# Optimization experiments

Hardware: AMD Instinct MI355X
Metric: run time of the kernel (lower is better)

Reference implementation:

```python
import jax, jax.numpy as jnp
import numpy as np

B = 64
C = 384
HEADS = 6
HD = 64
MLP = 1536
LAYERS = 12
PATCH = 16
IMG = 224
GRID = IMG // PATCH  # 14
NPATCH = GRID * GRID  # 196
NCLS = 100
EPS = 1e-6
PRUNE = {2: 0.1, 4: 0.15, 6: 0.2}
SCALE = HD ** -0.5


def layer_norm(x, g, b):
    m = jnp.mean(x, axis=-1, keepdims=True)
    v = jnp.var(x, axis=-1, keepdims=True)
    return (x - m) * jax.lax.rsqrt(v + EPS) * g + b


def attention(x, qkv_w, qkv_b, proj_w, proj_b):
    # x: [B, N, C]; weights stored as [in, out]
    Bn, N, _ = x.shape
    qkv = x @ qkv_w + qkv_b                      # [B, N, 3C]
    qkv = qkv.reshape(Bn, N, 3, HEADS, HD).transpose(2, 0, 3, 1, 4)
    q, k, v = qkv[0], qkv[1], qkv[2]             # [B, H, N, HD]
    attn = jax.nn.softmax(jnp.einsum('bhnd,bhmd->bhnm', q, k) * SCALE, axis=-1)
    out = jnp.einsum('bhnm,bhmd->bhnd', attn, v)
    out = out.transpose(0, 2, 1, 3).reshape(Bn, N, C)
    return out @ proj_w + proj_b, attn


def mlp(x, fc1_w, fc1_b, fc2_w, fc2_b):
    h = jax.nn.gelu(x @ fc1_w + fc1_b, approximate=False)
    return h @ fc2_w + fc2_b


def prune(x, attn, ratio):
    # x: [B, N, C]; attn: [B, H, N, N]
    scores = attn[:, :, 0, 1:].mean(axis=1)      # CLS attention to tokens, head-avg [B, N-1]
    keep = int(scores.shape[1] * (1 - ratio))
    _, idx = jax.lax.top_k(scores, keep)         # [B, keep], descending score order (matches torch.topk)
    tokens = jnp.take_along_axis(x[:, 1:, :], idx[:, :, None], axis=1)
    return jnp.concatenate([x[:, :1, :], tokens], axis=1)


def patch_embed(x, patch_w, patch_b):
    # 16x16 stride-16 conv == patchify + matmul. x: [B, 3, 224, 224]
    Bn = x.shape[0]
    p = x.reshape(Bn, 3, GRID, PATCH, GRID, PATCH).transpose(0, 2, 4, 1, 3, 5)
    p = p.reshape(Bn, NPATCH, 3 * PATCH * PATCH)
    return p @ patch_w + patch_b


def setup_inputs() -> dict:
    key = jax.random.key(0)
    ks = jax.random.split(key, 10)
    s = 0.02
    d = {}
    d['x'] = jax.random.normal(ks[0], (B, 3, IMG, IMG), jnp.float32)
    d['patch_w'] = jax.random.normal(ks[1], (3 * PATCH * PATCH, C), jnp.float32) * s
    d['patch_b'] = jnp.zeros((C,), jnp.float32)
    d['cls_token'] = jax.random.normal(ks[2], (1, 1, C), jnp.float32) * s
    d['pos_embed'] = jax.random.normal(ks[3], (1, NPATCH + 1, C), jnp.float32) * s
    d['ln1_g'] = jnp.ones((LAYERS, C), jnp.float32)
    d['ln1_b'] = jnp.zeros((LAYERS, C), jnp.float32)
    d['qkv_w'] = jax.random.normal(ks[4], (LAYERS, C, 3 * C), jnp.float32) * s
    d['qkv_b'] = jnp.zeros((LAYERS, 3 * C), jnp.float32)
    d['proj_w'] = jax.random.normal(ks[5], (LAYERS, C, C), jnp.float32) * s
    d['proj_b'] = jnp.zeros((LAYERS, C), jnp.float32)
    d['ln2_g'] = jnp.ones((LAYERS, C), jnp.float32)
    d['ln2_b'] = jnp.zeros((LAYERS, C), jnp.float32)
    d['fc1_w'] = jax.random.normal(ks[6], (LAYERS, C, MLP), jnp.float32) * s
    d['fc1_b'] = jnp.zeros((LAYERS, MLP), jnp.float32)
    d['fc2_w'] = jax.random.normal(ks[7], (LAYERS, MLP, C), jnp.float32) * s
    d['fc2_b'] = jnp.zeros((LAYERS, C), jnp.float32)
    d['norm_g'] = jnp.ones((C,), jnp.float32)
    d['norm_b'] = jnp.zeros((C,), jnp.float32)
    d['head_w'] = jax.random.normal(ks[8], (C, NCLS), jnp.float32) * s
    d['head_b'] = jnp.zeros((NCLS,), jnp.float32)
    return d


def reference(x, patch_w, patch_b, cls_token, pos_embed, ln1_g, ln1_b, qkv_w, qkv_b,
              proj_w, proj_b, ln2_g, ln2_b, fc1_w, fc1_b, fc2_w, fc2_b,
              norm_g, norm_b, head_w, head_b):
    Bn = x.shape[0]
    h = patch_embed(x, patch_w, patch_b)                          # [B, 196, C]
    cls = jnp.broadcast_to(cls_token, (Bn, 1, C))
    h = jnp.concatenate([cls, h], axis=1) + pos_embed             # [B, 197, C]
    for i in range(LAYERS):
        y, attn = attention(layer_norm(h, ln1_g[i], ln1_b[i]),
                            qkv_w[i], qkv_b[i], proj_w[i], proj_b[i])
        h = h + y
        if i in PRUNE:
            h = prune(h, attn, PRUNE[i])
        h = h + mlp(layer_norm(h, ln2_g[i], ln2_b[i]),
                    fc1_w[i], fc1_b[i], fc2_w[i], fc2_b[i])
    h = layer_norm(h, norm_g, norm_b)
    return h[:, 0] @ head_w + head_b                              # [B, NCLS]
```

## Files before the change

### kernel.cpp

```cpp
#include <hip/hip_runtime.h>
#include <hip/hip_bf16.h>
#include <math.h>

#define BATCH 64
#define CDIM 384
#define NHEADS 6
#define HD 64
#define MLPD 1536
#define NLAYERS 12
#define NPATCH 196
#define NTOK0 197
#define NCLS 100

typedef unsigned short ushortT;
typedef __attribute__((ext_vector_type(8))) short short8v;
typedef __attribute__((ext_vector_type(4))) float float4v;

__device__ inline ushortT f2b(float f) {
  union { float f; unsigned u; } x; x.f = f;
  unsigned r = x.u + 0x7fffu + ((x.u >> 16) & 1u);
  return (ushortT)(r >> 16);
}
__device__ inline float b2f(ushortT u) {
  union { unsigned u; float f; } x; x.u = ((unsigned)u) << 16;
  return x.f;
}

__device__ inline void gload_lds16(const ushortT* g, ushortT* l) {
  __builtin_amdgcn_global_load_lds((const __attribute__((address_space(1))) void*)g,
                                   (__attribute__((address_space(3))) void*)l, 16, 0, 0);
}

__device__ inline float wave_sum(float v) {
  #pragma unroll
  for (int o = 32; o > 0; o >>= 1) v += __shfl_xor(v, o);
  return v;
}

__global__ __launch_bounds__(256) void im2col_bf16(const float* __restrict__ x, ushortT* __restrict__ P) {
  int i = blockIdx.x * 256 + threadIdx.x;
  const int total = BATCH * NPATCH * 768;
  if (i >= total) return;
  int k = i % 768;
  int row = i / 768;
  int c = k >> 8;
  int r = k & 255;
  int py = r >> 4, px = r & 15;
  int b = row / NPATCH;
  int p = row % NPATCH;
  int gy = p / 14, gx = p % 14;
  P[i] = f2b(x[(((size_t)b * 3 + c) * 224 + gy * 16 + py) * 224 + gx * 16 + px]);
}

__global__ __launch_bounds__(256) void assemble_kernel(const float* __restrict__ patchout,
                                                       const float* __restrict__ cls_tok,
                                                       const float* __restrict__ pos,
                                                       float* __restrict__ h) {
  int i = blockIdx.x * 256 + threadIdx.x;
  const int total = BATCH * NTOK0 * CDIM;
  if (i >= total) return;
  int c = i % CDIM;
  int n = (i / CDIM) % NTOK0;
  int b = i / (CDIM * NTOK0);
  float v = (n == 0) ? cls_tok[c] : patchout[((size_t)b * NPATCH + (n - 1)) * CDIM + c];
  h[i] = v + pos[n * CDIM + c];
}

__global__ __launch_bounds__(256) void wtrans_layer(const float* __restrict__ qkv_w, const float* __restrict__ proj_w,
                                                    const float* __restrict__ fc1_w, const float* __restrict__ fc2_w,
                                                    ushortT* __restrict__ wq, ushortT* __restrict__ wp,
                                                    ushortT* __restrict__ w1, ushortT* __restrict__ w2) {
  int id = blockIdx.x;
  const float* W; ushortT* O; int K, N, t;
  if (id < 432)       { W = qkv_w; O = wq; K = 384;  N = 1152; t = id; }
  else if (id < 576)  { W = proj_w; O = wp; K = 384; N = 384;  t = id - 432; }
  else if (id < 1152) { W = fc1_w; O = w1; K = 384;  N = 1536; t = id - 576; }
  else                { W = fc2_w; O = w2; K = 1536; N = 384;  t = id - 1152; }
  int tilesK = K >> 5;
  int k0 = (t % tilesK) << 5, n0 = (t / tilesK) << 5;
  __shared__ float tile[32][33];
  int tx = threadIdx.x & 31, ty = threadIdx.x >> 5;
  #pragma unroll
  for (int i = 0; i < 4; ++i)
    tile[ty + 8 * i][tx] = W[(size_t)(k0 + ty + 8 * i) * N + n0 + tx];
  __syncthreads();
  #pragma unroll
  for (int i = 0; i < 4; ++i)
    O[(size_t)(n0 + ty + 8 * i) * K + k0 + tx] = f2b(tile[tx][ty + 8 * i]);
}

__global__ __launch_bounds__(256) void wtrans_one(const float* __restrict__ W, ushortT* __restrict__ O, int K, int N) {
  int t = blockIdx.x;
  int tilesK = K >> 5;
  int k0 = (t % tilesK) << 5, n0 = (t / tilesK) << 5;
  __shared__ float tile[32][33];
  int tx = threadIdx.x & 31, ty = threadIdx.x >> 5;
  #pragma unroll
  for (int i = 0; i < 4; ++i)
    tile[ty + 8 * i][tx] = W[(size_t)(k0 + ty + 8 * i) * N + n0 + tx];
  __syncthreads();
  #pragma unroll
  for (int i = 0; i < 4; ++i)
    O[(size_t)(n0 + ty + 8 * i) * K + k0 + tx] = f2b(tile[tx][ty + 8 * i]);
}

template<int ACT, int RES, int OBF>
__global__ __launch_bounds__(256) void gemm_mfma(const ushortT* __restrict__ A, const ushortT* __restrict__ Wt,
                                                 const float* __restrict__ bias, const float* __restrict__ res,
                                                 void* __restrict__ outp, int M, int N, int K) {
  __shared__ __align__(16) ushortT Asl[128 * 32];
  __shared__ __align__(16) ushortT Bsl[128 * 32];
  const int tid = threadIdx.x;
  const int lane = tid & 63, wave = tid >> 6;
  const int wr = wave >> 1, wc = wave & 1;
  const int bm = blockIdx.y * 128, bn = blockIdx.x * 128;
  float4v acc[4][4] = {};

  const int srow = wave * 16 + (lane >> 2);
  const int scol = (lane & 3) * 8;
  const ushortT* ag0 = A + (size_t)(bm + srow) * K + scol;
  const ushortT* ag1 = A + (size_t)(bm + 64 + srow) * K + scol;
  const ushortT* bg0 = Wt + (size_t)(bn + srow) * K + scol;
  const ushortT* bg1 = Wt + (size_t)(bn + 64 + srow) * K + scol;
  ushortT* ldsA0 = &Asl[wave * 512];
  ushortT* ldsA1 = &Asl[2048 + wave * 512];
  ushortT* ldsB0 = &Bsl[wave * 512];
  ushortT* ldsB1 = &Bsl[2048 + wave * 512];

  const int fr = lane & 15, g8 = (lane >> 4) * 8;

  for (int k0 = 0; k0 < K; k0 += 32) {
    gload_lds16(ag0 + k0, ldsA0);
    gload_lds16(ag1 + k0, ldsA1);
    gload_lds16(bg0 + k0, ldsB0);
    gload_lds16(bg1 + k0, ldsB1);
    __syncthreads();
    short8v af[4], bf[4];
    #pragma unroll
    for (int i = 0; i < 4; ++i) {
      af[i] = *(const short8v*)&Asl[(wr * 64 + i * 16 + fr) * 32 + g8];
      bf[i] = *(const short8v*)&Bsl[(wc * 64 + i * 16 + fr) * 32 + g8];
    }
    #pragma unroll
    for (int i = 0; i < 4; ++i)
      #pragma unroll
      for (int j = 0; j < 4; ++j)
        acc[i][j] = __builtin_amdgcn_mfma_f32_16x16x32_bf16(af[i], bf[j], acc[i][j], 0, 0, 0);
    __syncthreads();
  }

  const int c0 = lane & 15;
  const int r4 = (lane >> 4) * 4;
  #pragma unroll
  for (int i = 0; i < 4; ++i) {
    #pragma unroll
    for (int j = 0; j < 4; ++j) {
      const int col = bn + wc * 64 + j * 16 + c0;
      #pragma unroll
      for (int q = 0; q < 4; ++q) {
        const int row = bm + wr * 64 + i * 16 + r4 + q;
        if (row < M) {
          float v = acc[i][j][q] + bias[col];
          if (ACT == 1) v = 0.5f * v * (1.0f + erff(v * 0.70710678118654752f));
          if (RES) v += res[(size_t)row * N + col];
          if (OBF) ((ushortT*)outp)[(size_t)row * N + col] = f2b(v);
          else     ((float*)outp)[(size_t)row * N + col] = v;
        }
      }
    }
  }
}

__global__ __launch_bounds__(256) void ln_bf16(const float* __restrict__ in, ushortT* __restrict__ out,
                                               const float* __restrict__ g, const float* __restrict__ bb,
                                               int rows) {
  const int r = blockIdx.x * 4 + (threadIdx.x >> 6);
  if (r >= rows) return;
  const int t = threadIdx.x & 63;
  const float* xr = in + (size_t)r * CDIM;
  ushortT* orow = out + (size_t)r * CDIM;
  float v[6];
  float s = 0.f;
  #pragma unroll
  for (int i = 0; i < 6; ++i) { v[i] = xr[i * 64 + t]; s += v[i]; }
  s = wave_sum(s);
  float mean = s * (1.0f / CDIM);
  float q = 0.f;
  #pragma unroll
  for (int i = 0; i < 6; ++i) { float d = v[i] - mean; q += d * d; }
  q = wave_sum(q);
  float rstd = rsqrtf(q * (1.0f / CDIM) + 1e-6f);
  #pragma unroll
  for (int i = 0; i < 6; ++i) {
    int c = i * 64 + t;
    orow[c] = f2b((v[i] - mean) * rstd * g[c] + bb[c]);
  }
}

__global__ __launch_bounds__(64) void ln_kernel(const float* __restrict__ in, float* __restrict__ out,
                                                const float* __restrict__ g, const float* __restrict__ bb,
                                                int rows, size_t in_stride, size_t out_stride) {
  int r = blockIdx.x;
  if (r >= rows) return;
  const float* xr = in + (size_t)r * in_stride;
  float* orow = out + (size_t)r * out_stride;
  int t = threadIdx.x;
  float v[6];
  float s = 0.f;
  #pragma unroll
  for (int i = 0; i < 6; ++i) { v[i] = xr[i * 64 + t]; s += v[i]; }
  s = wave_sum(s);
  float mean = s * (1.0f / CDIM);
  float q = 0.f;
  #pragma unroll
  for (int i = 0; i < 6; ++i) { float d = v[i] - mean; q += d * d; }
  q = wave_sum(q);
  float rstd = rsqrtf(q * (1.0f / CDIM) + 1e-6f);
  #pragma unroll
  for (int i = 0; i < 6; ++i) {
    int c = i * 64 + t;
    orow[c] = (v[i] - mean) * rstd * g[c] + bb[c];
  }
}

template<int KS>
__global__ __launch_bounds__(256) void attn3(const ushortT* __restrict__ qkv, ushortT* __restrict__ attnout,
                                             float* __restrict__ cls_attn, int N) {
  constexpr int NT = 2 * KS;
  constexpr int KT = 32 * KS;
  const int h = blockIdx.y, b = blockIdx.z;
  const int rb = blockIdx.x * 64;
  const int tid = threadIdx.x;
  const int w = tid >> 6, l = tid & 63;
  const int c = l & 15, g = l >> 4;

  __shared__ __align__(16) ushortT Vt[64][232];
  __shared__ __align__(16) ushortT Ps[4][16][232];

  const ushortT* bq = qkv + (size_t)(b * N) * 1152 + (size_t)h * 64;

  {
    const int vr = tid >> 3, vc = (tid & 7) * 8;
    for (int p = 0; p < KT; p += 32) {
      const int m = vr + p;
      if (m < N) {
        short8v v8 = *(const short8v*)(bq + (size_t)m * 1152 + 768 + vc);
        #pragma unroll
        for (int j = 0; j < 8; ++j) Vt[vc + j][m] = (ushortT)v8[j];
      } else if (m < KT) {
        #pragma unroll
        for (int j = 0; j < 8; ++j) Vt[vc + j][m] = 0;
      }
    }
  }
  __syncthreads();

  short8v qf0, qf1;
  {
    int row = rb + 16 * w + c; if (row >= N) row = N - 1;
    const ushortT* qrow = bq + (size_t)row * 1152;
    qf0 = *(const short8v*)(qrow + g * 8);
    qf1 = *(const short8v*)(qrow + 32 + g * 8);
  }

  float4v sc[NT];
  #pragma unroll
  for (int kt = 0; kt < NT; ++kt) {
    int krow = 16 * kt + c; if (krow >= N) krow = N - 1;
    const ushortT* kr = bq + (size_t)krow * 1152 + 384;
    short8v b0 = *(const short8v*)(kr + g * 8);
    short8v b1 = *(const short8v*)(kr + 32 + g * 8);
    float4v a = {};
    a = __builtin_amdgcn_mfma_f32_16x16x32_bf16(qf0, b0, a, 0, 0, 0);
    a = __builtin_amdgcn_mfma_f32_16x16x32_bf16(qf1, b1, a, 0, 0, 0);
    sc[kt] = a;
  }

  float m4[4] = {-INFINITY, -INFINITY, -INFINITY, -INFINITY};
  #pragma unroll
  for (int kt = 0; kt < NT; ++kt) {
    const bool valid = (16 * kt + c) < N;
    #pragma unroll
    for (int q = 0; q < 4; ++q) {
      float s = valid ? sc[kt][q] * 0.125f : -INFINITY;
      sc[kt][q] = s;
      m4[q] = fmaxf(m4[q], s);
    }
  }
  #pragma unroll
  for (int q = 0; q < 4; ++q) {
    #pragma unroll
    for (int o = 1; o <= 8; o <<= 1) m4[q] = fmaxf(m4[q], __shfl_xor(m4[q], o));
  }
  float sum4[4] = {0.f, 0.f, 0.f, 0.f};
  #pragma unroll
  for (int kt = 0; kt < NT; ++kt) {
    #pragma unroll
    for (int q = 0; q < 4; ++q) {
      float e = __expf(sc[kt][q] - m4[q]);
      sc[kt][q] = e;
      sum4[q] += e;
    }
  }
  #pragma unroll
  for (int q = 0; q < 4; ++q) {
    #pragma unroll
    for (int o = 1; o <= 8; o <<= 1) sum4[q] += __shfl_xor(sum4[q], o);
  }
  float inv4[4];
  #pragma unroll
  for (int q = 0; q < 4; ++q) inv4[q] = 1.0f / sum4[q];

  #pragma unroll
  for (int kt = 0; kt < NT; ++kt) {
    #pragma unroll
    for (int q = 0; q < 4; ++q) Ps[w][4 * g + q][16 * kt + c] = f2b(sc[kt][q]);
  }

  if (rb == 0 && w == 0 && g == 0) {
    const float inv0 = inv4[0];
    #pragma unroll
    for (int kt = 0; kt < NT; ++kt) {
      const int col = 16 * kt + c;
      if (col >= 1 && col < N)
        cls_attn[((size_t)b * NHEADS + h) * (N - 1) + (col - 1)] = sc[kt][0] * inv0;
    }
  }

  float4v oacc[4] = {};
  #pragma unroll
  for (int s2 = 0; s2 < KS; ++s2) {
    short8v pa = *(const short8v*)&Ps[w][c][32 * s2 + 8 * g];
    #pragma unroll
    for (int nt = 0; nt < 4; ++nt) {
      short8v vb = *(const short8v*)&Vt[16 * nt + c][32 * s2 + 8 * g];
      oacc[nt] = __builtin_amdgcn_mfma_f32_16x16x32_bf16(pa, vb, oacc[nt], 0, 0, 0);
    }
  }

  #pragma unroll
  for (int nt = 0; nt < 4; ++nt) {
    #pragma unroll
    for (int q = 0; q < 4; ++q) {
      const int row = rb + 16 * w + 4 * g + q;
      if (row < N)
        attnout[((size_t)(b * N + row)) * CDIM + h * 64 + 16 * nt + c] = f2b(oacc[nt][q] * inv4[q]);
    }
  }
}

__global__ __launch_bounds__(256) void topk_rank(const float* __restrict__ cls_attn, int* __restrict__ idx,
                                                 int Nm1, int Kkeep) {
  const int b = blockIdx.x;
  const int t = threadIdx.x;
  __shared__ float s_sc[224];
  if (t < Nm1) {
    const float* ca = cls_attn + (size_t)b * NHEADS * Nm1 + t;
    float s = 0.f;
    #pragma unroll
    for (int h = 0; h < NHEADS; ++h) s += ca[h * Nm1];
    s_sc[t] = s * (1.0f / NHEADS);
  }
  __syncthreads();
  if (t < Nm1) {
    const float mys = s_sc[t];
    int r = 0;
    for (int i = 0; i < Nm1; ++i) {
      float si = s_sc[i];
      r += (si > mys || (si == mys && i < t)) ? 1 : 0;
    }
    if (r < Kkeep) idx[b * Kkeep + r] = t;
  }
}

__global__ __launch_bounds__(256) void gather_kernel(const float* __restrict__ h, const int* __restrict__ idx,
                                                     float* __restrict__ outb, int N, int Kkeep) {
  size_t total = (size_t)BATCH * (1 + Kkeep) * CDIM;
  size_t i = (size_t)blockIdx.x * 256 + threadIdx.x;
  if (i >= total) return;
  int c = (int)(i % CDIM);
  size_t r = i / CDIM;
  int n = (int)(r % (1 + Kkeep));
  int b = (int)(r / (1 + Kkeep));
  int src = (n == 0) ? 0 : 1 + idx[b * Kkeep + (n - 1)];
  outb[i] = h[((size_t)b * N + src) * CDIM + c];
}

__global__ __launch_bounds__(256) void gemm_f32(const float* __restrict__ A, const float* __restrict__ W,
                                                const float* __restrict__ bias, float* __restrict__ out,
                                                int M, int N, int K) {
  __shared__ __align__(16) float As[16][64];
  __shared__ __align__(16) float Ws[16][64];
  const int tid = threadIdx.x;
  const int tx = tid & 15, ty = tid >> 4;
  const int bm = blockIdx.y * 64, bn = blockIdx.x * 64;
  float acc[4][4] = {};
  const int ma = tid >> 2;
  const int ka = (tid & 3) << 2;
  const int kw = ty;
  const int nw = tx << 2;
  for (int k0 = 0; k0 < K; k0 += 16) {
    {
      float4 a4 = make_float4(0.f, 0.f, 0.f, 0.f);
      if (bm + ma < M) a4 = *reinterpret_cast<const float4*>(&A[(size_t)(bm + ma) * K + k0 + ka]);
      As[ka + 0][ma] = a4.x; As[ka + 1][ma] = a4.y; As[ka + 2][ma] = a4.z; As[ka + 3][ma] = a4.w;
    }
    {
      const int gn = bn + nw;
      const float* wp = &W[(size_t)(k0 + kw) * N + gn];
      #pragma unroll
      for (int j = 0; j < 4; ++j) Ws[kw][nw + j] = (gn + j < N) ? wp[j] : 0.f;
    }
    __syncthreads();
    #pragma unroll
    for (int kk = 0; kk < 16; ++kk) {
      float4 a = *reinterpret_cast<const float4*>(&As[kk][ty << 2]);
      float4 w = *reinterpret_cast<const float4*>(&Ws[kk][tx << 2]);
      float av[4] = {a.x, a.y, a.z, a.w};
      float wv[4] = {w.x, w.y, w.z, w.w};
      #pragma unroll
      for (int i = 0; i < 4; ++i)
        #pragma unroll
        for (int j = 0; j < 4; ++j)
          acc[i][j] = fmaf(av[i], wv[j], acc[i][j]);
    }
    __syncthreads();
  }
  #pragma unroll
  for (int i = 0; i < 4; ++i) {
    int r = bm + (ty << 2) + i;
    if (r >= M) continue;
    #pragma unroll
    for (int j = 0; j < 4; ++j) {
      int cidx = bn + (tx << 2) + j;
      if (cidx >= N) continue;
      out[(size_t)r * N + cidx] = acc[i][j] + bias[cidx];
    }
  }
}

extern "C" void kernel_launch(void* const* d_in, const int* in_sizes, int n_in,
                              void* d_out, int out_size, void* d_ws, size_t ws_size,
                              hipStream_t stream) {
  const float* x        = (const float*)d_in[0];
  const float* patch_w  = (const float*)d_in[1];
  const float* patch_b  = (const float*)d_in[2];
  const float* cls_tok  = (const float*)d_in[3];
  const float* pos      = (const float*)d_in[4];
  const float* ln1_g    = (const float*)d_in[5];
  const float* ln1_b    = (const float*)d_in[6];
  const float* qkv_w    = (const float*)d_in[7];
  const float* qkv_b    = (const float*)d_in[8];
  const float* proj_w   = (const float*)d_in[9];
  const float* proj_b   = (const float*)d_in[10];
  const float* ln2_g    = (const float*)d_in[11];
  const float* ln2_b    = (const float*)d_in[12];
  const float* fc1_w    = (const float*)d_in[13];
  const float* fc1_b    = (const float*)d_in[14];
  const float* fc2_w    = (const float*)d_in[15];
  const float* fc2_b    = (const float*)d_in[16];
  const float* norm_g   = (const float*)d_in[17];
  const float* norm_b   = (const float*)d_in[18];
  const float* head_w   = (const float*)d_in[19];
  const float* head_b   = (const float*)d_in[20];
  float* out = (float*)d_out;

  float* ws = (float*)d_ws;
  float* hA       = ws;
  float* big      = ws + 4841472;
  ushortT* big_u  = (ushortT*)big;
  float* patchout = big + 4816896;
  float* hB       = ws + 14524416;
  ushortT* lnb_u  = (ushortT*)(ws + 19365888);
  ushortT* attn_u = (ushortT*)(ws + 21786624);
  ushortT* wbuf_u = (ushortT*)(ws + 24207360);
  float* cls_attn = ws + 25092096;
  int*   idxbuf   = (int*)(ws + 25179904);
  float* cls0     = ws + 25191168;

  ushortT* wq = wbuf_u;
  ushortT* wp = wbuf_u + 442368;
  ushortT* w1 = wbuf_u + 589824;
  ushortT* w2 = wbuf_u + 1179648;

  {
    int total = BATCH * NPATCH * 768;
    im2col_bf16<<<(total + 255) / 256, 256, 0, stream>>>(x, big_u);
    wtrans_one<<<288, 256, 0, stream>>>(patch_w, wbuf_u, 768, CDIM);
    gemm_mfma<0, 0, 0><<<dim3(3, 98), 256, 0, stream>>>(big_u, wbuf_u, patch_b, nullptr, patchout,
                                                        BATCH * NPATCH, CDIM, 768);
    int tot2 = BATCH * NTOK0 * CDIM;
    assemble_kernel<<<(tot2 + 255) / 256, 256, 0, stream>>>(patchout, cls_tok, pos, hA);
  }

  float* h = hA;
  float* hOther = hB;
  int ncur = NTOK0;
  for (int i = 0; i < NLAYERS; ++i) {
    int M = BATCH * ncur;
    int gy = (M + 127) / 128;
    wtrans_layer<<<1728, 256, 0, stream>>>(qkv_w + (size_t)i * CDIM * 3 * CDIM,
                                           proj_w + (size_t)i * CDIM * CDIM,
                                           fc1_w + (size_t)i * CDIM * MLPD,
                                           fc2_w + (size_t)i * MLPD * CDIM,
                                           wq, wp, w1, w2);
    ln_bf16<<<(M + 3) / 4, 256, 0, stream>>>(h, lnb_u, ln1_g + i * CDIM, ln1_b + i * CDIM, M);
    gemm_mfma<0, 0, 1><<<dim3(9, gy), 256, 0, stream>>>(lnb_u, wq, qkv_b + i * 3 * CDIM, nullptr,
                                                        big_u, M, 3 * CDIM, CDIM);
    {
      dim3 g((ncur + 63) / 64, NHEADS, BATCH);
      int ks = (ncur + 31) / 32;
      if (ks == 7)      attn3<7><<<g, 256, 0, stream>>>(big_u, attn_u, cls_attn, ncur);
      else if (ks == 6) attn3<6><<<g, 256, 0, stream>>>(big_u, attn_u, cls_attn, ncur);
      else if (ks == 5) attn3<5><<<g, 256, 0, stream>>>(big_u, attn_u, cls_attn, ncur);
      else              attn3<4><<<g, 256, 0, stream>>>(big_u, attn_u, cls_attn, ncur);
    }
    gemm_mfma<0, 1, 0><<<dim3(3, gy), 256, 0, stream>>>(attn_u, wp, proj_b + i * CDIM, h,
                                                        h, M, CDIM, CDIM);
    if (i == 2 || i == 4 || i == 6) {
      int keep = (i == 2) ? 176 : (i == 4) ? 149 : 119;
      int Nm1 = ncur - 1;
      topk_rank<<<BATCH, 256, 0, stream>>>(cls_attn, idxbuf, Nm1, keep);
      int newN = 1 + keep;
      size_t gtot = (size_t)BATCH * newN * CDIM;
      gather_kernel<<<(int)((gtot + 255) / 256), 256, 0, stream>>>(h, idxbuf, hOther, ncur, keep);
      float* tmp = h; h = hOther; hOther = tmp;
      ncur = newN;
      M = BATCH * ncur;
      gy = (M + 127) / 128;
    }
    ln_bf16<<<(M + 3) / 4, 256, 0, stream>>>(h, lnb_u, ln2_g + i * CDIM, ln2_b + i * CDIM, M);
    gemm_mfma<1, 0, 1><<<dim3(12, gy), 256, 0, stream>>>(lnb_u, w1, fc1_b + i * MLPD, nullptr,
                                                         big_u, M, MLPD, CDIM);
    gemm_mfma<0, 1, 0><<<dim3(3, gy), 256, 0, stream>>>(big_u, w2, fc2_b + i * CDIM, h,
                                                        h, M, CDIM, MLPD);
  }

  ln_kernel<<<BATCH, 64, 0, stream>>>(h, cls0, norm_g, norm_b, BATCH, (size_t)ncur * CDIM, CDIM);
  gemm_f32<<<dim3(2, 1), 256, 0, stream>>>(cls0, head_w, head_b, out, BATCH, NCLS, CDIM);
}
```

Measured before the change: 2.751 ms.

## Double-buffer GEMM LDS tiles and remap workgroups across XCDs

The MFMA GEMM now uses two LDS buffers per operand, so the next K tile is prefetched while the current one feeds the MFMAs, dropping one barrier per iteration. The grid is flattened to 1D, and block IDs are remapped so consecutive tiles land on the same XCD for better L2 sharing. This doubles LDS use (occupancy risk) and relies on the barrier draining the async global-to-LDS loads.

New measurement: 2.451 ms. 10.9% less time.

```diff
diff --git a/kernel.cpp b/kernel.cpp
--- a/kernel.cpp
+++ b/kernel.cpp
@@ -107,13 +107,20 @@
 template<int ACT, int RES, int OBF>
 __global__ __launch_bounds__(256) void gemm_mfma(const ushortT* __restrict__ A, const ushortT* __restrict__ Wt,
                                                  const float* __restrict__ bias, const float* __restrict__ res,
-                                                 void* __restrict__ outp, int M, int N, int K) {
-  __shared__ __align__(16) ushortT Asl[128 * 32];
-  __shared__ __align__(16) ushortT Bsl[128 * 32];
+                                                 void* __restrict__ outp, int M, int N, int K, int gx) {
+  __shared__ __align__(16) ushortT Asl[2][4096];
+  __shared__ __align__(16) ushortT Bsl[2][4096];
   const int tid = threadIdx.x;
   const int lane = tid & 63, wave = tid >> 6;
   const int wr = wave >> 1, wc = wave & 1;
-  const int bm = blockIdx.y * 128, bn = blockIdx.x * 128;
+
+  const int nwg = gridDim.x;
+  const int orig = blockIdx.x;
+  const int q = nwg >> 3, r = nwg & 7;
+  const int xcd = orig & 7;
+  const int wgid = (xcd < r ? xcd * (q + 1) : r * (q + 1) + (xcd - r) * q) + (orig >> 3);
+  const int bm = (wgid / gx) * 128, bn = (wgid % gx) * 128;
+
   float4v acc[4][4] = {};
 
   const int srow = wave * 16 + (lane >> 2);
@@ -122,31 +129,41 @@
   const ushortT* ag1 = A + (size_t)(bm + 64 + srow) * K + scol;
   const ushortT* bg0 = Wt + (size_t)(bn + srow) * K + scol;
   const ushortT* bg1 = Wt + (size_t)(bn + 64 + srow) * K + scol;
-  ushortT* ldsA0 = &Asl[wave * 512];
-  ushortT* ldsA1 = &Asl[2048 + wave * 512];
-  ushortT* ldsB0 = &Bsl[wave * 512];
-  ushortT* ldsB1 = &Bsl[2048 + wave * 512];
 
   const int fr = lane & 15, g8 = (lane >> 4) * 8;
-
-  for (int k0 = 0; k0 < K; k0 += 32) {
-    gload_lds16(ag0 + k0, ldsA0);
-    gload_lds16(ag1 + k0, ldsA1);
-    gload_lds16(bg0 + k0, ldsB0);
-    gload_lds16(bg1 + k0, ldsB1);
-    __syncthreads();
+  const int nt = K >> 5;
+
+  gload_lds16(ag0, &Asl[0][wave * 512]);
+  gload_lds16(ag1, &Asl[0][2048 + wave * 512]);
+  gload_lds16(bg0, &Bsl[0][wave * 512]);
+  gload_lds16(bg1, &Bsl[0][2048 + wave * 512]);
+  __syncthreads();
+
+  int cur = 0;
+  for (int t = 0; t < nt; ++t) {
+    if (t + 1 < nt) {
+      const int k0 = (t + 1) << 5;
+      const int nxt = cur ^ 1;
+      gload_lds16(ag0 + k0, &Asl[nxt][wave * 512]);
+      gload_lds16(ag1 + k0, &Asl[nxt][2048 + wave * 512]);
+      gload_lds16(bg0 + k0, &Bsl[nxt][wave * 512]);
+      gload_lds16(bg1 + k0, &Bsl[nxt][2048 + wave * 512]);
+    }
     short8v af[4], bf[4];
     #pragma unroll
     for (int i = 0; i < 4; ++i) {
-      af[i] = *(const short8v*)&Asl[(wr * 64 + i * 16 + fr) * 32 + g8];
-      bf[i] = *(const short8v*)&Bsl[(wc * 64 + i * 16 + fr) * 32 + g8];
+      af[i] = *(const short8v*)&Asl[cur][(wr * 64 + i * 16 + fr) * 32 + g8];
+      bf[i] = *(const short8v*)&Bsl[cur][(wc * 64 + i * 16 + fr) * 32 + g8];
     }
     #pragma unroll
     for (int i = 0; i < 4; ++i)
       #pragma unroll
       for (int j = 0; j < 4; ++j)
         acc[i][j] = __builtin_amdgcn_mfma_f32_16x16x32_bf16(af[i], bf[j], acc[i][j], 0, 0, 0);
-    __syncthreads();
+    if (t + 1 < nt) {
+      __syncthreads();
+      cur ^= 1;
+    }
   }
 
   const int c0 = lane & 15;
@@ -157,10 +174,10 @@
     for (int j = 0; j < 4; ++j) {
       const int col = bn + wc * 64 + j * 16 + c0;
       #pragma unroll
-      for (int q = 0; q < 4; ++q) {
-        const int row = bm + wr * 64 + i * 16 + r4 + q;
+      for (int qq = 0; qq < 4; ++qq) {
+        const int row = bm + wr * 64 + i * 16 + r4 + qq;
         if (row < M) {
-          float v = acc[i][j][q] + bias[col];
+          float v = acc[i][j][qq] + bias[col];
           if (ACT == 1) v = 0.5f * v * (1.0f + erff(v * 0.70710678118654752f));
           if (RES) v += res[(size_t)row * N + col];
           if (OBF) ((ushortT*)outp)[(size_t)row * N + col] = f2b(v);
@@ -487,8 +504,8 @@
     int total = BATCH * NPATCH * 768;
     im2col_bf16<<<(total + 255) / 256, 256, 0, stream>>>(x, big_u);
     wtrans_one<<<288, 256, 0, stream>>>(patch_w, wbuf_u, 768, CDIM);
-    gemm_mfma<0, 0, 0><<<dim3(3, 98), 256, 0, stream>>>(big_u, wbuf_u, patch_b, nullptr, patchout,
-                                                        BATCH * NPATCH, CDIM, 768);
+    gemm_mfma<0, 0, 0><<<3 * 98, 256, 0, stream>>>(big_u, wbuf_u, patch_b, nullptr, patchout,
+                                                   BATCH * NPATCH, CDIM, 768, 3);
     int tot2 = BATCH * NTOK0 * CDIM;
     assemble_kernel<<<(tot2 + 255) / 256, 256, 0, stream>>>(patchout, cls_tok, pos, hA);
   }
@@ -505,8 +522,8 @@
                                            fc2_w + (size_t)i * MLPD * CDIM,
                                            wq, wp, w1, w2);
     ln_bf16<<<(M + 3) / 4, 256, 0, stream>>>(h, lnb_u, ln1_g + i * CDIM, ln1_b + i * CDIM, M);
-    gemm_mfma<0, 0, 1><<<dim3(9, gy), 256, 0, stream>>>(lnb_u, wq, qkv_b + i * 3 * CDIM, nullptr,
-                                                        big_u, M, 3 * CDIM, CDIM);
+    gemm_mfma<0, 0, 1><<<9 * gy, 256, 0, stream>>>(lnb_u, wq, qkv_b + i * 3 * CDIM, nullptr,
+                                                   big_u, M, 3 * CDIM, CDIM, 9);
     {
       dim3 g((ncur + 63) / 64, NHEADS, BATCH);
       int ks = (ncur + 31) / 32;
@@ -515,8 +532,8 @@
       else if (ks == 5) attn3<5><<<g, 256, 0, stream>>>(big_u, attn_u, cls_attn, ncur);
       else              attn3<4><<<g, 256, 0, stream>>>(big_u, attn_u, cls_attn, ncur);
     }
-    gemm_mfma<0, 1, 0><<<dim3(3, gy), 256, 0, stream>>>(attn_u, wp, proj_b + i * CDIM, h,
-                                                        h, M, CDIM, CDIM);
+    gemm_mfma<0, 1, 0><<<3 * gy, 256, 0, stream>>>(attn_u, wp, proj_b + i * CDIM, h,
+                                                   h, M, CDIM, CDIM, 3);
     if (i == 2 || i == 4 || i == 6) {
       int keep = (i == 2) ? 176 : (i == 4) ? 149 : 119;
       int Nm1 = ncur - 1;
@@ -530,10 +547,10 @@
       gy = (M + 127) / 128;
     }
     ln_bf16<<<(M + 3) / 4, 256, 0, stream>>>(h, lnb_u, ln2_g + i * CDIM, ln2_b + i * CDIM, M);
-    gemm_mfma<1, 0, 1><<<dim3(12, gy), 256, 0, stream>>>(lnb_u, w1, fc1_b + i * MLPD, nullptr,
-                                                         big_u, M, MLPD, CDIM);
-    gemm_mfma<0, 1, 0><<<dim3(3, gy), 256, 0, stream>>>(big_u, w2, fc2_b + i * CDIM, h,
-                                                        h, M, CDIM, MLPD);
+    gemm_mfma<1, 0, 1><<<12 * gy, 256, 0, stream>>>(lnb_u, w1, fc1_b + i * MLPD, nullptr,
+                                                    big_u, M, MLPD, CDIM, 12);
+    gemm_mfma<0, 1, 0><<<3 * gy, 256, 0, stream>>>(big_u, w2, fc2_b + i * CDIM, h,
+                                                   h, M, CDIM, MLPD, 3);
   }
 
   ln_kernel<<<BATCH, 64, 0, stream>>>(h, cls0, norm_g, norm_b, BATCH, (size_t)ncur * CDIM, CDIM);
```
